# Kernel tuning notes

Hardware: AMD Instinct MI355X
Metric: run time of the kernel (lower is better)

The kernel has to match this reference:

```python
import jax, jax.numpy as jnp
import numpy as np

SMOOTHING = 0.9  # NEURON_CONFIG['signal_smoothing']
NUM_SOURCE = 16384
NUM_TARGET = 16384
NUM_BRANCHES = 64
BATCH = 32


def setup_inputs() -> dict:
    key = jax.random.key(0)
    k1, k2, k3, k4 = jax.random.split(key, 4)
    spikes = jax.random.normal(k1, (BATCH, NUM_SOURCE), dtype=jnp.float32)
    attenuation = jax.random.uniform(k2, (NUM_SOURCE, NUM_BRANCHES), dtype=jnp.float32)
    target_indices = jax.random.randint(k3, (NUM_SOURCE, NUM_BRANCHES), 0, NUM_TARGET)
    delays = jax.random.randint(k4, (NUM_SOURCE, NUM_BRANCHES), 0, 6)
    return {"spikes": spikes, "attenuation": attenuation,
            "target_indices": target_indices, "delays": delays}


def reference(spikes, attenuation, target_indices, delays):
    # spikes: [B, S]; attenuation/delays/target_indices: [S, Br]
    B = spikes.shape[0]
    num_target = NUM_TARGET
    att = jnp.clip(attenuation, 0.0, 1.0)
    decay = SMOOTHING ** delays.astype(spikes.dtype)          # [S, Br]
    # fused elementwise: signal per (batch, source, branch)
    signals = spikes[:, :, None] * (att * decay)[None, :, :]   # [B, S, Br]
    flat_t = target_indices.reshape(-1)                        # [S*Br]
    flat_s = signals.reshape(B, -1)                            # [B, S*Br]
    out = jnp.zeros((B, num_target), dtype=spikes.dtype)
    out = out.at[jnp.arange(B)[:, None], flat_t[None, :]].add(flat_s)
    return out
```

## Files before the change

kernel.cpp:

```cpp
#include <hip/hip_runtime.h>

#define S_   16384
#define T_   16384
#define B_   32
#define NEDGES (S_ * 64)
#define GP_  512
#define EPG  2048
#define NBKT 512
#define TPB  32
#define CAP_SRT 2432

__device__ __forceinline__ float edge_weight(float a, int d) {
  float w = fminf(fmaxf(a, 0.0f), 1.0f);
  float r = (d & 1) ? 0.9f : 1.0f;
  r = (d & 2) ? r * 0.81f   : r;
  r = (d & 4) ? r * 0.6561f : r;
  return w * r;
}

__global__ __launch_bounds__(512) void produce(
    const float* __restrict__ spikes,
    const float* __restrict__ att,
    const int*   __restrict__ tgt,
    const int*   __restrict__ del,
    float*    __restrict__ spikesT,
    int2*     __restrict__ rec,
    unsigned* __restrict__ cntg,
    unsigned* __restrict__ ofse) {
  __shared__ float tile[32][33];
  __shared__ int4  sbuf4[EPG / 2];
  __shared__ unsigned cntp[4096];
  __shared__ unsigned short tofs[16384];
  __shared__ int wtot[8];
  int2* buf = (int2*)sbuf4;

  const int g = blockIdx.x, tid = threadIdx.x;
#pragma unroll
  for (int i = 0; i < 8; ++i) cntp[tid + 512 * i] = 0u;

  const int s0 = g * 32;
  {
    const int x = tid & 31, y = tid >> 5;
    tile[x][y]      = spikes[(size_t)y        * S_ + s0 + x];
    tile[x][y + 16] = spikes[(size_t)(y + 16) * S_ + s0 + x];
  }

  const int e4 = g * 512 + tid;
  int4   t = reinterpret_cast<const int4*>(tgt)[e4];
  float4 a = reinterpret_cast<const float4*>(att)[e4];
  int4   d = reinterpret_cast<const int4*>(del)[e4];
  const int src = e4 >> 4;

  __syncthreads();

  {
    const int b = tid & 31, j = tid >> 5;
    spikesT[(size_t)(s0 + j)      * 32 + b] = tile[j][b];
    spikesT[(size_t)(s0 + j + 16) * 32 + b] = tile[j + 16][b];
  }

  int r0, r1, r2, r3;
  {
    unsigned o;
    o = __hip_atomic_fetch_add(&cntp[t.x >> 2], 1u << (8 * (t.x & 3)),
                               __ATOMIC_RELAXED, __HIP_MEMORY_SCOPE_WORKGROUP);
    r0 = (int)((o >> (8 * (t.x & 3))) & 0xFF);
    o = __hip_atomic_fetch_add(&cntp[t.y >> 2], 1u << (8 * (t.y & 3)),
                               __ATOMIC_RELAXED, __HIP_MEMORY_SCOPE_WORKGROUP);
    r1 = (int)((o >> (8 * (t.y & 3))) & 0xFF);
    o = __hip_atomic_fetch_add(&cntp[t.z >> 2], 1u << (8 * (t.z & 3)),
                               __ATOMIC_RELAXED, __HIP_MEMORY_SCOPE_WORKGROUP);
    r2 = (int)((o >> (8 * (t.z & 3))) & 0xFF);
    o = __hip_atomic_fetch_add(&cntp[t.w >> 2], 1u << (8 * (t.w & 3)),
                               __ATOMIC_RELAXED, __HIP_MEMORY_SCOPE_WORKGROUP);
    r3 = (int)((o >> (8 * (t.w & 3))) & 0xFF);
  }
  __syncthreads();

  unsigned w[8];
  int tot = 0;
#pragma unroll
  for (int i = 0; i < 8; ++i) {
    w[i] = cntp[tid * 8 + i];
    tot += (w[i] & 0xFF) + ((w[i] >> 8) & 0xFF) + ((w[i] >> 16) & 0xFF) + (w[i] >> 24);
  }
  int incl = tot;
#pragma unroll
  for (int off = 1; off < 64; off <<= 1) {
    int u = __shfl_up(incl, off);
    if ((tid & 63) >= off) incl += u;
  }
  if ((tid & 63) == 63) wtot[tid >> 6] = incl;
  __syncthreads();
  int base = 0;
  for (int i = 0; i < (tid >> 6); ++i) base += wtot[i];
  const int start = base + incl - tot;
  int run = start;
#pragma unroll
  for (int i = 0; i < 8; ++i) {
#pragma unroll
    for (int bb = 0; bb < 4; ++bb) {
      tofs[tid * 32 + i * 4 + bb] = (unsigned short)run;
      run += (w[i] >> (8 * bb)) & 0xFF;
    }
  }
  ofse[(size_t)g * NBKT + tid] = ((unsigned)run << 16) | (unsigned)start;
#pragma unroll
  for (int i = 0; i < 8; ++i)
    cntg[(size_t)g * 4096 + tid + 512 * i] = cntp[tid + 512 * i];
  __syncthreads();

#define PUT(TT, RK, AV, DV)                                                   \
  {                                                                           \
    const int p = (int)tofs[TT] + (RK);                                       \
    buf[p] = make_int2((((RK) & 31) << 19) | (((TT) & 31) << 14) | src,       \
                       __float_as_int(edge_weight((AV), (DV))));              \
  }
  PUT(t.x, r0, a.x, d.x)
  PUT(t.y, r1, a.y, d.y)
  PUT(t.z, r2, a.z, d.z)
  PUT(t.w, r3, a.w, d.w)
#undef PUT
  __syncthreads();

  int4* recO = reinterpret_cast<int4*>(rec) + (size_t)g * (EPG / 2);
  recO[tid]       = sbuf4[tid];
  recO[tid + 512] = sbuf4[tid + 512];
}

__global__ __launch_bounds__(512) void consume(
    const int2*     __restrict__ rec,
    const unsigned* __restrict__ ofse,
    const unsigned* __restrict__ cntg,
    const float*    __restrict__ spikesT,
    float* __restrict__ out) {
  __shared__ int2  srt[CAP_SRT];
  __shared__ unsigned cw[GP_][9];
  __shared__ unsigned short lpos[TPB][GP_ + 2];
  __shared__ unsigned short prt[16][TPB];
  __shared__ unsigned short ttot[TPB];
  __shared__ float otile[TPB][33];
  __shared__ unsigned sse[GP_];
  __shared__ int ofs[TPB + 1];

  const int k = blockIdx.x, tid = threadIdx.x;
  const int b = tid & 31, hw = tid >> 5;

  sse[tid] = ofse[(size_t)tid * NBKT + k];
  {
    const uint4* cp = reinterpret_cast<const uint4*>(cntg + (size_t)tid * 4096 + k * 8);
    uint4 c0 = cp[0], c1 = cp[1];
    cw[tid][0] = c0.x; cw[tid][1] = c0.y; cw[tid][2] = c0.z; cw[tid][3] = c0.w;
    cw[tid][4] = c1.x; cw[tid][5] = c1.y; cw[tid][6] = c1.z; cw[tid][7] = c1.w;
  }
  __syncthreads();

  const int wd = b >> 2, sh = 8 * (b & 3);
  {
    int s = 0;
    for (int j = 0; j < 32; ++j) s += (cw[hw * 32 + j][wd] >> sh) & 0xFF;
    prt[hw][b] = (unsigned short)s;
  }
  __syncthreads();
  {
    int pbase = 0;
    for (int c = 0; c < hw; ++c) pbase += prt[c][b];
    int run = pbase;
    for (int j = 0; j < 32; ++j) {
      lpos[b][hw * 32 + j] = (unsigned short)run;
      run += (cw[hw * 32 + j][wd] >> sh) & 0xFF;
    }
    if (hw == 15) ttot[b] = (unsigned short)run;
  }
  __syncthreads();
  if (tid < 32) {
    int v = ttot[tid], ii = v;
#pragma unroll
    for (int off = 1; off < 32; off <<= 1) {
      int u = __shfl_up(ii, off);
      if (tid >= off) ii += u;
    }
    ofs[tid] = ii - v;
    if (tid == 31) ofs[32] = ii;
  }
  __syncthreads();

  const int sub = b >> 3, j0 = b & 7;
  for (int it = 0; it < 8; ++it) {
    const int g = it * 64 + hw * 4 + sub;
    const unsigned u = sse[g];
    const int st = (int)(u & 0xFFFF);
    const int n  = (int)(u >> 16) - st;
    const int2* slice = rec + (size_t)g * EPG + st;
    for (int j = j0; j < n; j += 8) {
      int2 r = slice[j];
      const int tl  = (r.x >> 14) & 31;
      const int rk  = (r.x >> 19) & 31;
      const int idx = ofs[tl] + (int)lpos[tl][g] + rk;
      if (idx < CAP_SRT) srt[idx] = r;
    }
  }
  __syncthreads();

  float acc0 = 0.f, acc1 = 0.f;
  {
    int e        = min(ofs[hw], CAP_SRT);
    const int e1 = min(ofs[hw + 1], CAP_SRT);
    for (; e + 4 <= e1; e += 4) {
      int2 q0 = srt[e], q1 = srt[e + 1], q2 = srt[e + 2], q3 = srt[e + 3];
      float f0 = spikesT[(size_t)(q0.x & 0x3FFF) * 32 + b];
      float f1 = spikesT[(size_t)(q1.x & 0x3FFF) * 32 + b];
      float f2 = spikesT[(size_t)(q2.x & 0x3FFF) * 32 + b];
      float f3 = spikesT[(size_t)(q3.x & 0x3FFF) * 32 + b];
      acc0 = fmaf(__int_as_float(q0.y), f0, acc0);
      acc0 = fmaf(__int_as_float(q1.y), f1, acc0);
      acc0 = fmaf(__int_as_float(q2.y), f2, acc0);
      acc0 = fmaf(__int_as_float(q3.y), f3, acc0);
    }
    for (; e < e1; ++e) {
      int2 q = srt[e];
      acc0 = fmaf(__int_as_float(q.y), spikesT[(size_t)(q.x & 0x3FFF) * 32 + b], acc0);
    }
  }
  {
    int e        = min(ofs[hw + 16], CAP_SRT);
    const int e1 = min(ofs[hw + 17], CAP_SRT);
    for (; e + 4 <= e1; e += 4) {
      int2 q0 = srt[e], q1 = srt[e + 1], q2 = srt[e + 2], q3 = srt[e + 3];
      float f0 = spikesT[(size_t)(q0.x & 0x3FFF) * 32 + b];
      float f1 = spikesT[(size_t)(q1.x & 0x3FFF) * 32 + b];
      float f2 = spikesT[(size_t)(q2.x & 0x3FFF) * 32 + b];
      float f3 = spikesT[(size_t)(q3.x & 0x3FFF) * 32 + b];
      acc1 = fmaf(__int_as_float(q0.y), f0, acc1);
      acc1 = fmaf(__int_as_float(q1.y), f1, acc1);
      acc1 = fmaf(__int_as_float(q2.y), f2, acc1);
      acc1 = fmaf(__int_as_float(q3.y), f3, acc1);
    }
    for (; e < e1; ++e) {
      int2 q = srt[e];
      acc1 = fmaf(__int_as_float(q.y), spikesT[(size_t)(q.x & 0x3FFF) * 32 + b], acc1);
    }
  }

  otile[hw][b]      = acc0;
  otile[hw + 16][b] = acc1;
  __syncthreads();
  const int bb = tid >> 4;
  const int cc = (tid & 15) * 2;
  float2 o2 = make_float2(otile[cc][bb], otile[cc + 1][bb]);
  *reinterpret_cast<float2*>(&out[(size_t)bb * T_ + k * 32 + cc]) = o2;
}

__global__ void zero_floats(float* __restrict__ p, int n) {
  int i = blockIdx.x * blockDim.x + threadIdx.x;
  if (i < n) p[i] = 0.0f;
}

__global__ void naive_kernel(const float* __restrict__ spikes,
                             const float* __restrict__ att,
                             const int*   __restrict__ tgt,
                             const int*   __restrict__ del,
                             float*       __restrict__ out) {
  int i = blockIdx.x * blockDim.x + threadIdx.x;
  if (i >= NEDGES) return;
  int   s = i >> 6;
  int   t = tgt[i];
  float w = edge_weight(att[i], del[i]);
  for (int b = 0; b < B_; ++b)
    unsafeAtomicAdd(&out[(size_t)b * T_ + t], w * spikes[(size_t)b * S_ + s]);
}

extern "C" void kernel_launch(void* const* d_in, const int* in_sizes, int n_in,
                              void* d_out, int out_size, void* d_ws, size_t ws_size,
                              hipStream_t stream) {
  const float* spikes = (const float*)d_in[0];
  const float* att    = (const float*)d_in[1];
  const int*   tgt    = (const int*)d_in[2];
  const int*   del    = (const int*)d_in[3];
  float*       out    = (float*)d_out;

  const size_t spikesT_bytes = (size_t)S_ * B_ * sizeof(float);
  const size_t rec_bytes     = (size_t)NEDGES * sizeof(int2);
  const size_t cnt_bytes     = (size_t)GP_ * 4096 * sizeof(unsigned);
  const size_t ofse_bytes    = (size_t)GP_ * NBKT * sizeof(unsigned);
  const size_t need = spikesT_bytes + rec_bytes + cnt_bytes + ofse_bytes + 64;

  if (ws_size < need) {
    zero_floats<<<(B_ * T_ + 255) / 256, 256, 0, stream>>>(out, B_ * T_);
    naive_kernel<<<(NEDGES + 255) / 256, 256, 0, stream>>>(spikes, att, tgt, del, out);
    return;
  }

  char* p = (char*)d_ws;
  float*    spikesT = (float*)p;    p += spikesT_bytes;
  int2*     rec     = (int2*)p;     p += rec_bytes;
  unsigned* cntg    = (unsigned*)p; p += cnt_bytes;
  unsigned* ofse    = (unsigned*)p;

  produce<<<GP_, 512, 0, stream>>>(spikes, att, tgt, del, spikesT, rec, cntg, ofse);
  consume<<<NBKT, 512, 0, stream>>>(rec, ofse, cntg, spikesT, out);
}
```

Measured before the change: 100.5 us.

## Drop global per-target count matrix; derive counts in consumer from sorted records

After: 109.8 us. 1.09x slower.

```diff
diff --git a/kernel.cpp b/kernel.cpp
--- a/kernel.cpp
+++ b/kernel.cpp
@@ -25,18 +25,17 @@
     const int*   __restrict__ del,
     float*    __restrict__ spikesT,
     int2*     __restrict__ rec,
-    unsigned* __restrict__ cntg,
     unsigned* __restrict__ ofse) {
   __shared__ float tile[32][33];
   __shared__ int4  sbuf4[EPG / 2];
   __shared__ unsigned cntp[4096];
-  __shared__ unsigned short tofs[16384];
-  __shared__ int wtot[8];
+  __shared__ int  sofs5[NBKT];
+  __shared__ int  wtot[8];
   int2* buf = (int2*)sbuf4;
 
   const int g = blockIdx.x, tid = threadIdx.x;
 #pragma unroll
-  for (int i = 0; i < 8; ++i) cntp[tid + 512 * i] = 0u;
+  for (int i = 0; i < 8; ++i) cntp[i * 512 + tid] = 0u;
 
   const int s0 = g * 32;
   {
@@ -59,30 +58,45 @@
     spikesT[(size_t)(s0 + j + 16) * 32 + b] = tile[j + 16][b];
   }
 
+#define SW(w) ((((w) & 7) << 9) | ((w) >> 3))
   int r0, r1, r2, r3;
   {
     unsigned o;
-    o = __hip_atomic_fetch_add(&cntp[t.x >> 2], 1u << (8 * (t.x & 3)),
+    o = __hip_atomic_fetch_add(&cntp[SW(t.x >> 2)], 1u << (8 * (t.x & 3)),
                                __ATOMIC_RELAXED, __HIP_MEMORY_SCOPE_WORKGROUP);
     r0 = (int)((o >> (8 * (t.x & 3))) & 0xFF);
-    o = __hip_atomic_fetch_add(&cntp[t.y >> 2], 1u << (8 * (t.y & 3)),
+    o = __hip_atomic_fetch_add(&cntp[SW(t.y >> 2)], 1u << (8 * (t.y & 3)),
                                __ATOMIC_RELAXED, __HIP_MEMORY_SCOPE_WORKGROUP);
     r1 = (int)((o >> (8 * (t.y & 3))) & 0xFF);
-    o = __hip_atomic_fetch_add(&cntp[t.z >> 2], 1u << (8 * (t.z & 3)),
+    o = __hip_atomic_fetch_add(&cntp[SW(t.z >> 2)], 1u << (8 * (t.z & 3)),
                                __ATOMIC_RELAXED, __HIP_MEMORY_SCOPE_WORKGROUP);
     r2 = (int)((o >> (8 * (t.z & 3))) & 0xFF);
-    o = __hip_atomic_fetch_add(&cntp[t.w >> 2], 1u << (8 * (t.w & 3)),
+    o = __hip_atomic_fetch_add(&cntp[SW(t.w >> 2)], 1u << (8 * (t.w & 3)),
                                __ATOMIC_RELAXED, __HIP_MEMORY_SCOPE_WORKGROUP);
     r3 = (int)((o >> (8 * (t.w & 3))) & 0xFF);
   }
   __syncthreads();
 
-  unsigned w[8];
+  unsigned wreg[8];
   int tot = 0;
 #pragma unroll
   for (int i = 0; i < 8; ++i) {
-    w[i] = cntp[tid * 8 + i];
-    tot += (w[i] & 0xFF) + ((w[i] >> 8) & 0xFF) + ((w[i] >> 16) & 0xFF) + (w[i] >> 24);
+    const unsigned c = cntp[i * 512 + tid];
+    wreg[i] = c;
+    tot += (c & 0xFF) + ((c >> 8) & 0xFF) + ((c >> 16) & 0xFF) + (c >> 24);
+  }
+  {
+    int run = 0;
+#pragma unroll
+    for (int i = 0; i < 8; ++i) {
+      unsigned rel = 0;
+#pragma unroll
+      for (int bb = 0; bb < 4; ++bb) {
+        rel |= (unsigned)run << (8 * bb);
+        run += (wreg[i] >> (8 * bb)) & 0xFF;
+      }
+      cntp[i * 512 + tid] = rel;
+    }
   }
   int incl = tot;
 #pragma unroll
@@ -92,27 +106,21 @@
   }
   if ((tid & 63) == 63) wtot[tid >> 6] = incl;
   __syncthreads();
-  int base = 0;
-  for (int i = 0; i < (tid >> 6); ++i) base += wtot[i];
-  const int start = base + incl - tot;
-  int run = start;
-#pragma unroll
-  for (int i = 0; i < 8; ++i) {
-#pragma unroll
-    for (int bb = 0; bb < 4; ++bb) {
-      tofs[tid * 32 + i * 4 + bb] = (unsigned short)run;
-      run += (w[i] >> (8 * bb)) & 0xFF;
-    }
-  }
-  ofse[(size_t)g * NBKT + tid] = ((unsigned)run << 16) | (unsigned)start;
-#pragma unroll
-  for (int i = 0; i < 8; ++i)
-    cntg[(size_t)g * 4096 + tid + 512 * i] = cntp[tid + 512 * i];
+  {
+    int base = 0;
+    for (int i = 0; i < (tid >> 6); ++i) base += wtot[i];
+    const int start = base + incl - tot;
+    sofs5[tid] = start;
+    ofse[(size_t)g * NBKT + tid] =
+        ((unsigned)(start + tot) << 16) | (unsigned)start;
+  }
   __syncthreads();
 
 #define PUT(TT, RK, AV, DV)                                                   \
   {                                                                           \
-    const int p = (int)tofs[TT] + (RK);                                       \
+    const unsigned relw = cntp[SW((TT) >> 2)];                                \
+    const int p = sofs5[(TT) >> 5] +                                          \
+                  (int)((relw >> (8 * ((TT) & 3))) & 0xFF) + (RK);            \
     buf[p] = make_int2((((RK) & 31) << 19) | (((TT) & 31) << 14) | src,       \
                        __float_as_int(edge_weight((AV), (DV))));              \
   }
@@ -121,6 +129,7 @@
   PUT(t.z, r2, a.z, d.z)
   PUT(t.w, r3, a.w, d.w)
 #undef PUT
+#undef SW
   __syncthreads();
 
   int4* recO = reinterpret_cast<int4*>(rec) + (size_t)g * (EPG / 2);
@@ -131,73 +140,102 @@
 __global__ __launch_bounds__(512) void consume(
     const int2*     __restrict__ rec,
     const unsigned* __restrict__ ofse,
-    const unsigned* __restrict__ cntg,
     const float*    __restrict__ spikesT,
     float* __restrict__ out) {
   __shared__ int2  srt[CAP_SRT];
-  __shared__ unsigned cw[GP_][9];
-  __shared__ unsigned short lpos[TPB][GP_ + 2];
-  __shared__ unsigned short prt[16][TPB];
-  __shared__ unsigned short ttot[TPB];
+  __shared__ unsigned short mat[TPB][GP_ + 2];
   __shared__ float otile[TPB][33];
   __shared__ unsigned sse[GP_];
+  __shared__ int prt[16][TPB + 1];
+  __shared__ int ttot[TPB];
   __shared__ int ofs[TPB + 1];
 
   const int k = blockIdx.x, tid = threadIdx.x;
   const int b = tid & 31, hw = tid >> 5;
-
+  const int sub = b >> 3, j0 = b & 7;
+
+  {
+    unsigned* m32 = (unsigned*)mat;
+    for (int i = tid; i < TPB * (GP_ + 2) / 2; i += 512) m32[i] = 0u;
+  }
   sse[tid] = ofse[(size_t)tid * NBKT + k];
-  {
-    const uint4* cp = reinterpret_cast<const uint4*>(cntg + (size_t)tid * 4096 + k * 8);
-    uint4 c0 = cp[0], c1 = cp[1];
-    cw[tid][0] = c0.x; cw[tid][1] = c0.y; cw[tid][2] = c0.z; cw[tid][3] = c0.w;
-    cw[tid][4] = c1.x; cw[tid][5] = c1.y; cw[tid][6] = c1.z; cw[tid][7] = c1.w;
-  }
-  __syncthreads();
-
-  const int wd = b >> 2, sh = 8 * (b & 3);
-  {
-    int s = 0;
-    for (int j = 0; j < 32; ++j) s += (cw[hw * 32 + j][wd] >> sh) & 0xFF;
-    prt[hw][b] = (unsigned short)s;
-  }
-  __syncthreads();
-  {
-    int pbase = 0;
-    for (int c = 0; c < hw; ++c) pbase += prt[c][b];
-    int run = pbase;
-    for (int j = 0; j < 32; ++j) {
-      lpos[b][hw * 32 + j] = (unsigned short)run;
-      run += (cw[hw * 32 + j][wd] >> sh) & 0xFF;
-    }
-    if (hw == 15) ttot[b] = (unsigned short)run;
-  }
-  __syncthreads();
-  if (tid < 32) {
-    int v = ttot[tid], ii = v;
-#pragma unroll
-    for (int off = 1; off < 32; off <<= 1) {
-      int u = __shfl_up(ii, off);
-      if (tid >= off) ii += u;
-    }
-    ofs[tid] = ii - v;
-    if (tid == 31) ofs[32] = ii;
-  }
-  __syncthreads();
-
-  const int sub = b >> 3, j0 = b & 7;
+  __syncthreads();
+
+  int2 rr[16];
+  int  nrec = 0;
+#pragma unroll
   for (int it = 0; it < 8; ++it) {
     const int g = it * 64 + hw * 4 + sub;
     const unsigned u = sse[g];
     const int st = (int)(u & 0xFFFF);
     const int n  = (int)(u >> 16) - st;
     const int2* slice = rec + (size_t)g * EPG + st;
-    for (int j = j0; j < n; j += 8) {
-      int2 r = slice[j];
-      const int tl  = (r.x >> 14) & 31;
-      const int rk  = (r.x >> 19) & 31;
-      const int idx = ofs[tl] + (int)lpos[tl][g] + rk;
-      if (idx < CAP_SRT) srt[idx] = r;
+    for (int c0 = 0; c0 < n; c0 += 8) {
+      const int j = c0 + j0;
+      int2 r = make_int2(0, 0);
+      if (j < n) r = slice[j];
+      const int nx = __shfl_down(r.x, 1);
+      if (j < n && nrec < 16) {
+        const int tl = (r.x >> 14) & 31;
+        bool last;
+        if (j + 1 >= n) last = true;
+        else if (j0 < 7) last = ((nx >> 14) & 31) != tl;
+        else             last = ((slice[j + 1].x >> 14) & 31) != tl;
+        if (last) mat[tl][g] = (unsigned short)(((r.x >> 19) & 31) + 1);
+        rr[nrec++] = r;
+      }
+    }
+  }
+  __syncthreads();
+
+  {
+    int s = 0;
+    for (int j = 0; j < 32; ++j) s += mat[b][hw * 32 + j];
+    prt[hw][b] = s;
+  }
+  __syncthreads();
+  {
+    int pbase = 0;
+    for (int c = 0; c < hw; ++c) pbase += prt[c][b];
+    int run = pbase;
+    for (int j = 0; j < 32; ++j) {
+      const int c = mat[b][hw * 32 + j];
+      mat[b][hw * 32 + j] = (unsigned short)run;
+      run += c;
+    }
+    if (hw == 15) ttot[b] = run;
+  }
+  __syncthreads();
+  if (tid < 32) {
+    int v = ttot[tid], ii = v;
+#pragma unroll
+    for (int off = 1; off < 32; off <<= 1) {
+      int u = __shfl_up(ii, off);
+      if (tid >= off) ii += u;
+    }
+    ofs[tid] = ii - v;
+    if (tid == 31) ofs[32] = ii;
+  }
+  __syncthreads();
+
+  {
+    int c = 0;
+#pragma unroll
+    for (int it = 0; it < 8; ++it) {
+      const int g = it * 64 + hw * 4 + sub;
+      const unsigned u = sse[g];
+      const int st = (int)(u & 0xFFFF);
+      const int n  = (int)(u >> 16) - st;
+      for (int c0 = 0; c0 < n; c0 += 8) {
+        const int j = c0 + j0;
+        if (j < n && c < 16) {
+          int2 r = rr[c++];
+          const int tl  = (r.x >> 14) & 31;
+          const int rk  = (r.x >> 19) & 31;
+          const int idx = ofs[tl] + (int)mat[tl][g] + rk;
+          if (idx < CAP_SRT) srt[idx] = r;
+        }
+      }
     }
   }
   __syncthreads();
@@ -281,9 +319,8 @@
 
   const size_t spikesT_bytes = (size_t)S_ * B_ * sizeof(float);
   const size_t rec_bytes     = (size_t)NEDGES * sizeof(int2);
-  const size_t cnt_bytes     = (size_t)GP_ * 4096 * sizeof(unsigned);
   const size_t ofse_bytes    = (size_t)GP_ * NBKT * sizeof(unsigned);
-  const size_t need = spikesT_bytes + rec_bytes + cnt_bytes + ofse_bytes + 64;
+  const size_t need = spikesT_bytes + rec_bytes + ofse_bytes + 64;
 
   if (ws_size < need) {
     zero_floats<<<(B_ * T_ + 255) / 256, 256, 0, stream>>>(out, B_ * T_);
@@ -294,9 +331,8 @@
   char* p = (char*)d_ws;
   float*    spikesT = (float*)p;    p += spikesT_bytes;
   int2*     rec     = (int2*)p;     p += rec_bytes;
-  unsigned* cntg    = (unsigned*)p; p += cnt_bytes;
   unsigned* ofse    = (unsigned*)p;
 
-  produce<<<GP_, 512, 0, stream>>>(spikes, att, tgt, del, spikesT, rec, cntg, ofse);
-  consume<<<NBKT, 512, 0, stream>>>(rec, ofse, cntg, spikesT, out);
-}
+  produce<<<GP_, 512, 0, stream>>>(spikes, att, tgt, del, spikesT, rec, ofse);
+  consume<<<NBKT, 512, 0, stream>>>(rec, ofse, spikesT, out);
+}
```
